# Kernel optimization log

Hardware: AMD Instinct MI355X
Metric: run time of the kernel (lower is better)

Reference implementation:

```python
import jax, jax.numpy as jnp
import numpy as np

NUM_HEADS = 8
KEY_DIM = 512      # total projected dim across heads
VALUE_DIM = 512
EMBED_DIM = 512


def setup_inputs() -> dict:
    key = jax.random.key(0)
    ks = jax.random.split(key, 12)
    B, S, E = 8, 1024, EMBED_DIM
    sc_in = 1.0 / np.sqrt(E)
    sc_o = 1.0 / np.sqrt(KEY_DIM)
    return {
        "queries": jax.random.normal(ks[0], (B, S, E), jnp.float32),
        "keys": jax.random.normal(ks[1], (B, S, E), jnp.float32),
        "values": jax.random.normal(ks[2], (B, S, E), jnp.float32),
        "Wq": jax.random.normal(ks[3], (E, KEY_DIM), jnp.float32) * sc_in,
        "bq": jnp.zeros((KEY_DIM,), jnp.float32),
        "Wk": jax.random.normal(ks[4], (E, KEY_DIM), jnp.float32) * sc_in,
        "bk": jnp.zeros((KEY_DIM,), jnp.float32),
        "Wv": jax.random.normal(ks[5], (E, VALUE_DIM), jnp.float32) * sc_in,
        "bv": jnp.zeros((VALUE_DIM,), jnp.float32),
        "Wo": jax.random.normal(ks[6], (KEY_DIM, EMBED_DIM), jnp.float32) * sc_o,
        "bo": jnp.zeros((EMBED_DIM,), jnp.float32),
    }


def _split_heads(x):
    # [B, S, key_dim] -> [B, H, S, key_dim//H]
    B, S, D = x.shape
    return x.reshape(B, S, NUM_HEADS, D // NUM_HEADS).transpose(0, 2, 1, 3)


def reference(queries, keys, values, Wq, bq, Wk, bk, Wv, bv, Wo, bo):
    q = _split_heads(queries @ Wq + bq)   # [B,H,S,dh]
    k = _split_heads(keys @ Wk + bk)
    v = _split_heads(values @ Wv + bv)
    # NOTE: original scales by sqrt(full key_dim), not per-head dim
    scores = jnp.einsum("bhqd,bhkd->bhqk", q, k) / jnp.sqrt(
        jnp.asarray(KEY_DIM, jnp.float32))
    weights = jax.nn.softmax(scores, axis=-1)
    o = jnp.einsum("bhqk,bhkd->bhqd", weights, v)  # [B,H,S,dh]
    B, H, S, dh = o.shape
    o = o.transpose(0, 2, 1, 3).reshape(B, S, H * dh)  # merge heads -> key_dim
    return o @ Wo + bo
```

## Files before the change

kernel.cpp:

```cpp
#include <hip/hip_runtime.h>


typedef __bf16 bf16x8 __attribute__((ext_vector_type(8)));
typedef __bf16 bf16x4 __attribute__((ext_vector_type(4)));
typedef float  f32x4  __attribute__((ext_vector_type(4)));

#define MFMA(a, b, c) __builtin_amdgcn_mfma_f32_16x16x32_bf16((a), (b), (c), 0, 0, 0)

#define WAITN_BAR(N) asm volatile("s_waitcnt vmcnt(" #N ")\n\ts_barrier" ::: "memory")

__device__ inline float fast_exp2(float x) {
  float r;
  asm("v_exp_f32 %0, %1" : "=v"(r) : "v"(x));
  return r;
}

__device__ inline bf16x8 cvt8(const float* p) {
  f32x4 u = *(const f32x4*)p;
  f32x4 v = *(const f32x4*)(p + 4);
  bf16x8 r;
  r[0] = (__bf16)u[0]; r[1] = (__bf16)u[1]; r[2] = (__bf16)u[2]; r[3] = (__bf16)u[3];
  r[4] = (__bf16)v[0]; r[5] = (__bf16)v[1]; r[6] = (__bf16)v[2]; r[7] = (__bf16)v[3];
  return r;
}

__device__ inline void gl_lds(const __bf16* g, __bf16* l) {
  __builtin_amdgcn_global_load_lds((const __attribute__((address_space(1))) void*)g,
                                   (__attribute__((address_space(3))) void*)l, 16, 0, 0);
}

__global__ __launch_bounds__(256) void cvt_qkv(const float* __restrict__ Q,
                                               const float* __restrict__ K,
                                               const float* __restrict__ V,
                                               __bf16* __restrict__ Qo,
                                               __bf16* __restrict__ Ko,
                                               __bf16* __restrict__ Vo) {
  const float* src;
  __bf16* dst;
  switch (blockIdx.y) {
    case 0: src = Q; dst = Qo; break;
    case 1: src = K; dst = Ko; break;
    default: src = V; dst = Vo; break;
  }
  const long idx = ((long)blockIdx.x * 256 + threadIdx.x) * 8;
  *(bf16x8*)(dst + idx) = cvt8(src + idx);
}

__global__ __launch_bounds__(256) void transpose_w4(const float* __restrict__ W0,
                                                    const float* __restrict__ W1,
                                                    const float* __restrict__ W2,
                                                    const float* __restrict__ W3,
                                                    __bf16* __restrict__ O0,
                                                    __bf16* __restrict__ O1,
                                                    __bf16* __restrict__ O2,
                                                    __bf16* __restrict__ O3,
                                                    float s0) {
  const float* in;
  __bf16* out;
  float sc = 1.0f;
  switch (blockIdx.y) {
    case 0: in = W0; out = O0; sc = s0; break;
    case 1: in = W1; out = O1; break;
    case 2: in = W2; out = O2; break;
    default: in = W3; out = O3; break;
  }
  __shared__ __align__(16) float t[64][65];
  const int tk = (blockIdx.x & 7) * 64;
  const int tn = (blockIdx.x >> 3) * 64;
  const int r0 = threadIdx.x >> 4;
  const int c4 = threadIdx.x & 15;
#pragma unroll
  for (int i = 0; i < 4; ++i) {
    int r = r0 + i * 16;
    f32x4 v = *(const f32x4*)(in + (long)(tk + r) * 512 + tn + c4 * 4);
#pragma unroll
    for (int j = 0; j < 4; ++j) t[r][c4 * 4 + j] = v[j] * sc;
  }
  __syncthreads();
  const int n0 = threadIdx.x >> 3;
  const int k8 = threadIdx.x & 7;
#pragma unroll
  for (int i = 0; i < 2; ++i) {
    int n = n0 + i * 32;
    bf16x8 v;
#pragma unroll
    for (int j = 0; j < 8; ++j) v[j] = (__bf16)t[k8 * 8 + j][n];
    *(bf16x8*)(out + (long)(tn + n) * 512 + tk + k8 * 8) = v;
  }
}

template <int MODE, typename OT>
__device__ __forceinline__ void gemm_core(const __bf16* __restrict__ X,
                                          const __bf16* __restrict__ Wt,
                                          const float* __restrict__ bias,
                                          OT* __restrict__ out, float bsc,
                                          char* smem) {
  __bf16* At = (__bf16*)smem;
  __bf16* Bt = (__bf16*)(smem + 24576);

  const int tid = threadIdx.x;
  const int lane = tid & 63, wid = tid >> 6, quad = lane >> 4, l16 = lane & 15;
  const int i = blockIdx.x;
  const int kk = i >> 3;
  const int bm = ((i & 7) * 8 + (kk >> 2)) * 128;
  const int bn = (kk & 3) * 128;
  const int wm = (wid >> 1) * 64;
  const int wn = (wid & 1) * 64;

  f32x4 acc[4][4] = {};

  const int rowB = lane >> 2;
  const int gB = (lane & 3) ^ ((rowB >> 1) & 3);

  auto stage = [&](int off, int k0) {
#pragma unroll
    for (int j = 0; j < 2; ++j) {
      const int g = wid * 2 + j;
      gl_lds(X + (long)(bm + g * 16 + rowB) * 512 + k0 + (gB << 3),
             &At[off + g * 512 + lane * 8]);
      gl_lds(Wt + (long)(bn + g * 16 + rowB) * 512 + k0 + (gB << 3),
             &Bt[off + g * 512 + lane * 8]);
    }
  };

  const int posm = quad ^ ((l16 >> 1) & 3);

  auto compute = [&](int co) {
    bf16x8 a[4], b[4];
#pragma unroll
    for (int t = 0; t < 4; ++t) {
      a[t] = *(const bf16x8*)(&At[co + (wm + t * 16 + l16) * 32 + (posm << 3)]);
      b[t] = *(const bf16x8*)(&Bt[co + (wn + t * 16 + l16) * 32 + (posm << 3)]);
    }
#pragma unroll
    for (int mt = 0; mt < 4; ++mt)
#pragma unroll
      for (int nt = 0; nt < 4; ++nt) acc[mt][nt] = MFMA(a[mt], b[nt], acc[mt][nt]);
  };

  stage(0, 0);
  stage(4096, 32);

  int co = 0, so = 8192;
  for (int c = 0; c < 15; ++c) {
    WAITN_BAR(4);
    if (c < 14) stage(so, (c + 2) * 32);
    compute(co);
    const int nc = 12288 - co - so;
    so = co;
    co = nc;
  }
  WAITN_BAR(0);
  compute(co);

  if constexpr (MODE == 4) {
    __syncthreads();
    __bf16* tb = (__bf16*)smem;
#pragma unroll
    for (int nt = 0; nt < 4; ++nt) {
      const int n = wn + nt * 16 + l16;
      const float bvv = bias[bn + n] * bsc;
#pragma unroll
      for (int mt = 0; mt < 4; ++mt) {
        const int m0 = wm + mt * 16 + quad * 4;
        bf16x4 w;
#pragma unroll
        for (int r = 0; r < 4; ++r) w[r] = (__bf16)(acc[mt][nt][r] + bvv);
        *(bf16x4*)(&tb[n * 128 + (((m0 >> 3) ^ (n & 15)) << 3) + (m0 & 7)]) = w;
      }
    }
    __syncthreads();
    const int nn = tid & 127, mhalf = tid >> 7;
    const int h = (bn + nn) >> 6;
    const int bb = bm >> 10;
    OT* ob = out + (long)(bb * 8 + h) * 65536;
    const int cbase = (bm & 1023) >> 6;
#pragma unroll
    for (int gi = 0; gi < 8; ++gi) {
      const int gl = mhalf * 8 + gi;
      bf16x8 v = *(const bf16x8*)(&tb[nn * 128 + ((gl ^ (nn & 15)) << 3)]);
      const long idx = ((((long)(cbase + (gl >> 3)) * 4 + ((nn >> 4) & 3)) * 2 +
                        ((gl >> 2) & 1)) * 64 + (gl & 3) * 16 + (nn & 15)) * 8;
      *(bf16x8*)(ob + idx) = v;
    }
    return;
  }

#pragma unroll
  for (int nt = 0; nt < 4; ++nt) {
    const int n = bn + wn + nt * 16 + l16;
    const float bvv = bias[n] * bsc;
    const int h = n >> 6, d = n & 63;
#pragma unroll
    for (int mt = 0; mt < 4; ++mt) {
#pragma unroll
      for (int r = 0; r < 4; ++r) {
        const int m = bm + wm + mt * 16 + quad * 4 + r;
        const float v = acc[mt][nt][r] + bvv;
        if constexpr (MODE == 0) {
          out[(long)m * 512 + n] = (OT)v;
        } else if constexpr (MODE == 1) {
          const int bb = m >> 10, s = m & 1023;
          out[((long)((bb * 8 + h) * 1024 + s)) * 64 + d] = (OT)v;
        } else {
          const int bb = m >> 10, s = m & 1023;
          const long idx = (long)(bb * 8 + h) * 65536 +
                           ((((s >> 6) * 4 + ((s >> 4) & 3)) * 2 + (d >> 5)) * 64 +
                            ((d >> 3) & 3) * 16 + (s & 15)) * 8 + (d & 7);
          out[idx] = (OT)v;
        }
      }
    }
  }
}

__global__ __launch_bounds__(256) void gemm_qkv(
    const __bf16* __restrict__ Qx, const __bf16* __restrict__ Kx,
    const __bf16* __restrict__ Vx, const __bf16* __restrict__ Wqt,
    const __bf16* __restrict__ Wkt, const __bf16* __restrict__ Wvt,
    const float* __restrict__ bq, const float* __restrict__ bk,
    const float* __restrict__ bv, __bf16* __restrict__ Qp,
    __bf16* __restrict__ Kp, __bf16* __restrict__ Vtp, float qscale) {
  __shared__ __align__(16) char smem[49152];
  if (blockIdx.y == 0)
    gemm_core<1, __bf16>(Qx, Wqt, bq, Qp, qscale, smem);
  else if (blockIdx.y == 1)
    gemm_core<3, __bf16>(Kx, Wkt, bk, Kp, 1.0f, smem);
  else
    gemm_core<4, __bf16>(Vx, Wvt, bv, Vtp, 1.0f, smem);
}

__global__ __launch_bounds__(256) void gemm_o(const __bf16* __restrict__ Oc,
                                              const __bf16* __restrict__ Wot,
                                              const float* __restrict__ bo,
                                              float* __restrict__ out) {
  __shared__ __align__(16) char smem[49152];
  gemm_core<0, float>(Oc, Wot, bo, out, 1.0f, smem);
}

__global__ __launch_bounds__(256, 2) void attn(const __bf16* __restrict__ Q,
                                               const __bf16* __restrict__ Kf,
                                               const __bf16* __restrict__ Vf,
                                               __bf16* __restrict__ Oc) {
  __shared__ __align__(16) __bf16 plds[4][2048];

  const int tid = threadIdx.x;
  const int lane = tid & 63, wid = tid >> 6, quad = lane >> 4, l16 = lane & 15;
  const int i = blockIdx.x;
  const int pair = (i & 7) + (((i >> 6) & 7) << 3);
  const int qt = (i >> 3) & 7;
  const int q0 = qt * 128 + wid * 32;
  const int b = pair >> 3, h = pair & 7;
  const int swz = l16 & 7;

  const __bf16* Qb = Q + (long)pair * 65536;
  const __bf16* Kb = Kf + (long)pair * 65536 + lane * 8;
  const __bf16* Vb = Vf + (long)pair * 65536 + lane * 8;
  __bf16* pw = plds[wid];

  bf16x8 bq[2][2];
#pragma unroll
  for (int t = 0; t < 2; ++t)
#pragma unroll
    for (int e = 0; e < 2; ++e)
      bq[t][e] = *(const bf16x8*)(Qb + (q0 + t * 16 + l16) * 64 + e * 32 + quad * 8);

  f32x4 lrv[2] = {};
  f32x4 oa[2][4] = {};

#define LOADK(dst, cc)                                                         \
  {                                                                            \
    _Pragma("unroll") for (int kt = 0; kt < 4; ++kt)                           \
        _Pragma("unroll") for (int e = 0; e < 2; ++e)                          \
            dst[kt][e] =                                                       \
        *(const bf16x8*)(Kb + ((((cc) * 4 + kt) * 2 + e) << 9));               \
  }

#define ABODY(kcur, knxt, cc)                                                  \
  {                                                                            \
    bf16x8 vf[4][2];                                                           \
    _Pragma("unroll") for (int nt = 0; nt < 4; ++nt)                           \
        _Pragma("unroll") for (int e = 0; e < 2; ++e)                          \
            vf[nt][e] =                                                        \
        *(const bf16x8*)(Vb + ((((cc) * 4 + nt) * 2 + e) << 9));               \
    f32x4 s[2][4] = {};                                                        \
    __builtin_amdgcn_s_setprio(1);                                             \
    _Pragma("unroll") for (int kt = 0; kt < 4; ++kt)                           \
        _Pragma("unroll") for (int t = 0; t < 2; ++t) {                        \
      s[t][kt] = MFMA(kcur[kt][0], bq[t][0], s[t][kt]);                        \
      s[t][kt] = MFMA(kcur[kt][1], bq[t][1], s[t][kt]);                        \
    }                                                                          \
    __builtin_amdgcn_s_setprio(0);                                             \
    if ((cc) < 15) LOADK(knxt, (cc) + 1);                                      \
    _Pragma("unroll") for (int t = 0; t < 2; ++t) {                            \
      const int prow = (t * 16 + l16) * 64;                                    \
      _Pragma("unroll") for (int kt = 0; kt < 4; ++kt) {                       \
        bf16x4 w;                                                              \
        _Pragma("unroll") for (int r = 0; r < 4; ++r) {                        \
          const float p = fast_exp2(s[t][kt][r]);                              \
          lrv[t][r] += p;                                                      \
          w[r] = (__bf16)p;                                                    \
        }                                                                      \
        *(bf16x4*)(&pw[prow + (((kt * 2 + (quad >> 1)) ^ swz) << 3) +          \
                       (quad & 1) * 4]) = w;                                   \
      }                                                                        \
    }                                                                          \
    bf16x8 pb[2][2];                                                           \
    _Pragma("unroll") for (int t = 0; t < 2; ++t)                              \
        _Pragma("unroll") for (int e = 0; e < 2; ++e)                          \
            pb[t][e] = *(const bf16x8*)(&pw[(t * 16 + l16) * 64 +              \
                                            (((e * 4 + quad) ^ swz) << 3)]);   \
    __builtin_amdgcn_s_setprio(1);                                             \
    _Pragma("unroll") for (int nt = 0; nt < 4; ++nt)                           \
        _Pragma("unroll") for (int t = 0; t < 2; ++t) {                        \
      oa[t][nt] = MFMA(vf[nt][0], pb[t][0], oa[t][nt]);                        \
      oa[t][nt] = MFMA(vf[nt][1], pb[t][1], oa[t][nt]);                        \
    }                                                                          \
    __builtin_amdgcn_s_setprio(0);                                             \
  }

  bf16x8 kA[4][2], kB[4][2];
  LOADK(kA, 0);
#pragma unroll 1
  for (int c = 0; c < 16; c += 2) {
    ABODY(kA, kB, c);
    ABODY(kB, kA, c + 1);
  }
#undef LOADK
#undef ABODY

#pragma unroll
  for (int t = 0; t < 2; ++t) {
    float lr = lrv[t][0] + lrv[t][1] + lrv[t][2] + lrv[t][3];
    lr += __shfl_xor(lr, 16);
    lr += __shfl_xor(lr, 32);
    const float inv = 1.0f / lr;
    const long base = ((long)b * 1024 + q0 + t * 16 + l16) * 512 + h * 64 + quad * 4;
#pragma unroll
    for (int nt = 0; nt < 4; ++nt) {
      bf16x4 w;
#pragma unroll
      for (int r = 0; r < 4; ++r) w[r] = (__bf16)(oa[t][nt][r] * inv);
      *(bf16x4*)(Oc + base + nt * 16) = w;
    }
  }
}

extern "C" void kernel_launch(void* const* d_in, const int* in_sizes, int n_in,
                              void* d_out, int out_size, void* d_ws, size_t ws_size,
                              hipStream_t stream) {
  const float* queries = (const float*)d_in[0];
  const float* keys = (const float*)d_in[1];
  const float* values = (const float*)d_in[2];
  const float* Wq = (const float*)d_in[3];
  const float* bq = (const float*)d_in[4];
  const float* Wk = (const float*)d_in[5];
  const float* bk = (const float*)d_in[6];
  const float* Wv = (const float*)d_in[7];
  const float* bv = (const float*)d_in[8];
  const float* Wo = (const float*)d_in[9];
  const float* bo = (const float*)d_in[10];
  float* out = (float*)d_out;

  __bf16* ws = (__bf16*)d_ws;
  const long WSZ = 512 * 512;
  const long XSZ = 8192L * 512;
  __bf16* Wqt = ws;
  __bf16* Wkt = ws + WSZ;
  __bf16* Wvt = ws + 2 * WSZ;
  __bf16* Wot = ws + 3 * WSZ;
  __bf16* Qp = ws + 4 * WSZ;
  __bf16* Kp = Qp + XSZ;
  __bf16* Vtp = Kp + XSZ;
  __bf16* Oc = Vtp + XSZ;
  __bf16* Qbf = Oc + XSZ;
  __bf16* Kbf = Qbf + XSZ;
  __bf16* Vbf = Kbf + XSZ;

  const float qscale = 0.044194173824159216f * 1.4426950408889634f;

  cvt_qkv<<<dim3(2048, 3), 256, 0, stream>>>(queries, keys, values, Qbf, Kbf, Vbf);
  transpose_w4<<<dim3(64, 4), 256, 0, stream>>>(Wq, Wk, Wv, Wo, Wqt, Wkt, Wvt, Wot,
                                                qscale);

  gemm_qkv<<<dim3(256, 3), 256, 0, stream>>>(Qbf, Kbf, Vbf, Wqt, Wkt, Wvt,
                                             bq, bk, bv, Qp, Kp, Vtp, qscale);

  attn<<<512, 256, 0, stream>>>(Qp, Kp, Vtp, Oc);

  gemm_o<<<256, 256, 0, stream>>>(Oc, Wot, bo, out);
}
```

Measured before the change: 162.1 us.

## Fuse fp32-to-bf16 input conversion into QKV projection GEMM loads

Removes the separate cvt_qkv kernel and has the QKV GEMM read fp32 activations directly into registers, convert them to bf16, and write them to LDS. The software pipeline is restructured with register double-buffering and explicit vmcnt waits, while weights still use direct global-to-LDS loads. This drops a full read and write pass of the bf16 activation copies plus one launch. In exchange the GEMM reads twice as many activation bytes, uses more registers, and does the conversion through VGPRs instead of async LDS loads.

New measurement: 171.4 us. +5.7%, slower.

```diff
diff --git a/kernel.cpp b/kernel.cpp
--- a/kernel.cpp
+++ b/kernel.cpp
@@ -15,9 +15,7 @@
   return r;
 }
 
-__device__ inline bf16x8 cvt8(const float* p) {
-  f32x4 u = *(const f32x4*)p;
-  f32x4 v = *(const f32x4*)(p + 4);
+__device__ inline bf16x8 cvt8r(f32x4 u, f32x4 v) {
   bf16x8 r;
   r[0] = (__bf16)u[0]; r[1] = (__bf16)u[1]; r[2] = (__bf16)u[2]; r[3] = (__bf16)u[3];
   r[4] = (__bf16)v[0]; r[5] = (__bf16)v[1]; r[6] = (__bf16)v[2]; r[7] = (__bf16)v[3];
@@ -27,23 +25,6 @@
 __device__ inline void gl_lds(const __bf16* g, __bf16* l) {
   __builtin_amdgcn_global_load_lds((const __attribute__((address_space(1))) void*)g,
                                    (__attribute__((address_space(3))) void*)l, 16, 0, 0);
-}
-
-__global__ __launch_bounds__(256) void cvt_qkv(const float* __restrict__ Q,
-                                               const float* __restrict__ K,
-                                               const float* __restrict__ V,
-                                               __bf16* __restrict__ Qo,
-                                               __bf16* __restrict__ Ko,
-                                               __bf16* __restrict__ Vo) {
-  const float* src;
-  __bf16* dst;
-  switch (blockIdx.y) {
-    case 0: src = Q; dst = Qo; break;
-    case 1: src = K; dst = Ko; break;
-    default: src = V; dst = Vo; break;
-  }
-  const long idx = ((long)blockIdx.x * 256 + threadIdx.x) * 8;
-  *(bf16x8*)(dst + idx) = cvt8(src + idx);
 }
 
 __global__ __launch_bounds__(256) void transpose_w4(const float* __restrict__ W0,
@@ -89,12 +70,13 @@
   }
 }
 
-template <int MODE, typename OT>
-__device__ __forceinline__ void gemm_core(const __bf16* __restrict__ X,
+template <int MODE, typename OT, typename XT>
+__device__ __forceinline__ void gemm_core(const XT* __restrict__ X,
                                           const __bf16* __restrict__ Wt,
                                           const float* __restrict__ bias,
                                           OT* __restrict__ out, float bsc,
                                           char* smem) {
+  constexpr bool F32X = (sizeof(XT) == 4);
   __bf16* At = (__bf16*)smem;
   __bf16* Bt = (__bf16*)(smem + 24576);
 
@@ -112,12 +94,10 @@
   const int rowB = lane >> 2;
   const int gB = (lane & 3) ^ ((rowB >> 1) & 3);
 
-  auto stage = [&](int off, int k0) {
+  auto wstage = [&](int off, int k0) {
 #pragma unroll
     for (int j = 0; j < 2; ++j) {
       const int g = wid * 2 + j;
-      gl_lds(X + (long)(bm + g * 16 + rowB) * 512 + k0 + (gB << 3),
-             &At[off + g * 512 + lane * 8]);
       gl_lds(Wt + (long)(bn + g * 16 + rowB) * 512 + k0 + (gB << 3),
              &Bt[off + g * 512 + lane * 8]);
     }
@@ -138,20 +118,81 @@
       for (int nt = 0; nt < 4; ++nt) acc[mt][nt] = MFMA(a[mt], b[nt], acc[mt][nt]);
   };
 
-  stage(0, 0);
-  stage(4096, 32);
-
-  int co = 0, so = 8192;
-  for (int c = 0; c < 15; ++c) {
-    WAITN_BAR(4);
-    if (c < 14) stage(so, (c + 2) * 32);
+  if constexpr (F32X) {
+    f32x4 xa[2][2], xb[2][2];
+    auto xload = [&](f32x4 (&dst)[2][2], int k0) {
+#pragma unroll
+      for (int j = 0; j < 2; ++j) {
+        const float* sp =
+            (const float*)X + (long)(bm + (wid * 2 + j) * 16 + rowB) * 512 + k0 + (gB << 3);
+        dst[j][0] = *(const f32x4*)sp;
+        dst[j][1] = *(const f32x4*)(sp + 4);
+      }
+    };
+    auto xwrite = [&](int off, const f32x4 (&src)[2][2]) {
+#pragma unroll
+      for (int j = 0; j < 2; ++j)
+        *(bf16x8*)(&At[off + (wid * 2 + j) * 512 + lane * 8]) =
+            cvt8r(src[j][0], src[j][1]);
+    };
+
+    xload(xa, 0);
+    wstage(0, 0);
+    asm volatile("" ::: "memory");
+    xload(xb, 32);
+    wstage(4096, 32);
+    asm volatile("s_waitcnt vmcnt(6)" ::: "memory");
+    xwrite(0, xa);
+
+    int co = 0, so = 8192;
+#pragma unroll 1
+    for (int c = 0; c < 14; c += 2) {
+      asm volatile("s_waitcnt vmcnt(6) lgkmcnt(0)\n\ts_barrier" ::: "memory");
+      xload(xa, (c + 2) * 32);
+      wstage(so, (c + 2) * 32);
+      asm volatile("s_waitcnt vmcnt(6)" ::: "memory");
+      xwrite(12288 - co - so, xb);
+      compute(co);
+      { const int nc = 12288 - co - so; so = co; co = nc; }
+      asm volatile("s_waitcnt vmcnt(6) lgkmcnt(0)\n\ts_barrier" ::: "memory");
+      xload(xb, (c + 3) * 32);
+      wstage(so, (c + 3) * 32);
+      asm volatile("s_waitcnt vmcnt(6)" ::: "memory");
+      xwrite(12288 - co - so, xa);
+      compute(co);
+      { const int nc = 12288 - co - so; so = co; co = nc; }
+    }
+    asm volatile("s_waitcnt vmcnt(6) lgkmcnt(0)\n\ts_barrier" ::: "memory");
+    asm volatile("s_waitcnt vmcnt(0)" ::: "memory");
+    xwrite(12288 - co - so, xb);
     compute(co);
-    const int nc = 12288 - co - so;
-    so = co;
-    co = nc;
-  }
-  WAITN_BAR(0);
-  compute(co);
+    { const int nc = 12288 - co - so; so = co; co = nc; }
+    asm volatile("s_waitcnt vmcnt(0) lgkmcnt(0)\n\ts_barrier" ::: "memory");
+    compute(co);
+  } else {
+    auto stage = [&](int off, int k0) {
+#pragma unroll
+      for (int j = 0; j < 2; ++j) {
+        const int g = wid * 2 + j;
+        gl_lds((const __bf16*)X + (long)(bm + g * 16 + rowB) * 512 + k0 + (gB << 3),
+               &At[off + g * 512 + lane * 8]);
+      }
+      wstage(off, k0);
+    };
+    stage(0, 0);
+    stage(4096, 32);
+    int co = 0, so = 8192;
+    for (int c = 0; c < 15; ++c) {
+      WAITN_BAR(4);
+      if (c < 14) stage(so, (c + 2) * 32);
+      compute(co);
+      const int nc = 12288 - co - so;
+      so = co;
+      co = nc;
+    }
+    WAITN_BAR(0);
+    compute(co);
+  }
 
   if constexpr (MODE == 4) {
     __syncthreads();
@@ -215,19 +256,19 @@
 }
 
 __global__ __launch_bounds__(256) void gemm_qkv(
-    const __bf16* __restrict__ Qx, const __bf16* __restrict__ Kx,
-    const __bf16* __restrict__ Vx, const __bf16* __restrict__ Wqt,
+    const float* __restrict__ Qx, const float* __restrict__ Kx,
+    const float* __restrict__ Vx, const __bf16* __restrict__ Wqt,
     const __bf16* __restrict__ Wkt, const __bf16* __restrict__ Wvt,
     const float* __restrict__ bq, const float* __restrict__ bk,
     const float* __restrict__ bv, __bf16* __restrict__ Qp,
     __bf16* __restrict__ Kp, __bf16* __restrict__ Vtp, float qscale) {
   __shared__ __align__(16) char smem[49152];
   if (blockIdx.y == 0)
-    gemm_core<1, __bf16>(Qx, Wqt, bq, Qp, qscale, smem);
+    gemm_core<1, __bf16, float>(Qx, Wqt, bq, Qp, qscale, smem);
   else if (blockIdx.y == 1)
-    gemm_core<3, __bf16>(Kx, Wkt, bk, Kp, 1.0f, smem);
+    gemm_core<3, __bf16, float>(Kx, Wkt, bk, Kp, 1.0f, smem);
   else
-    gemm_core<4, __bf16>(Vx, Wvt, bv, Vtp, 1.0f, smem);
+    gemm_core<4, __bf16, float>(Vx, Wvt, bv, Vtp, 1.0f, smem);
 }
 
 __global__ __launch_bounds__(256) void gemm_o(const __bf16* __restrict__ Oc,
@@ -235,7 +276,7 @@
                                               const float* __restrict__ bo,
                                               float* __restrict__ out) {
   __shared__ __align__(16) char smem[49152];
-  gemm_core<0, float>(Oc, Wot, bo, out, 1.0f, smem);
+  gemm_core<0, float, __bf16>(Oc, Wot, bo, out, 1.0f, smem);
 }
 
 __global__ __launch_bounds__(256, 2) void attn(const __bf16* __restrict__ Q,
@@ -373,17 +414,13 @@
   __bf16* Kp = Qp + XSZ;
   __bf16* Vtp = Kp + XSZ;
   __bf16* Oc = Vtp + XSZ;
-  __bf16* Qbf = Oc + XSZ;
-  __bf16* Kbf = Qbf + XSZ;
-  __bf16* Vbf = Kbf + XSZ;
 
   const float qscale = 0.044194173824159216f * 1.4426950408889634f;
 
-  cvt_qkv<<<dim3(2048, 3), 256, 0, stream>>>(queries, keys, values, Qbf, Kbf, Vbf);
   transpose_w4<<<dim3(64, 4), 256, 0, stream>>>(Wq, Wk, Wv, Wo, Wqt, Wkt, Wvt, Wot,
                                                 qscale);
 
-  gemm_qkv<<<dim3(256, 3), 256, 0, stream>>>(Qbf, Kbf, Vbf, Wqt, Wkt, Wvt,
+  gemm_qkv<<<dim3(256, 3), 256, 0, stream>>>(queries, keys, values, Wqt, Wkt, Wvt,
                                              bq, bk, bv, Qp, Kp, Vtp, qscale);
 
   attn<<<512, 256, 0, stream>>>(Qp, Kp, Vtp, Oc);
```
